# Kernel optimization log

Hardware: AMD Instinct MI355X
Metric: run time of the kernel (lower is better)

Reference implementation:

```python
import jax, jax.numpy as jnp
import numpy as np
import math

N_HEADS = 16
ROPE_THETA = 10000.0


def _rope_cos_sin(seqlen, head_dim, theta=ROPE_THETA):
    # freqs_cis = polar(1, outer(t, 1/theta^(2i/d))) -> return cos, sin parts
    inv = 1.0 / (theta ** (jnp.arange(0, head_dim, 2, dtype=jnp.float32) / head_dim))
    t = jnp.arange(seqlen, dtype=jnp.float32)
    freqs = t[:, None] * inv[None, :]          # [S, hd/2]
    return jnp.cos(freqs), jnp.sin(freqs)


def _apply_rope(x, cos, sin):
    # x: [B, S, H, hd]; treat consecutive pairs as complex, rotate by e^{i*freq}
    B, S, H, hd = x.shape
    x2 = x.astype(jnp.float32).reshape(B, S, H, hd // 2, 2)
    xr, xi = x2[..., 0], x2[..., 1]
    c = cos[None, :, None, :]
    s = sin[None, :, None, :]
    out_r = xr * c - xi * s
    out_i = xr * s + xi * c
    return jnp.stack([out_r, out_i], axis=-1).reshape(B, S, H, hd).astype(x.dtype)


def setup_inputs() -> dict:
    key = jax.random.key(0)
    ks = jax.random.split(key, 5)
    dim = 2048
    B, S = 2, 2048
    scale = 1.0 / math.sqrt(dim)
    x = jax.random.normal(ks[0], (B, S, dim), dtype=jnp.float32)
    wq = jax.random.normal(ks[1], (dim, dim), dtype=jnp.float32) * scale
    wk = jax.random.normal(ks[2], (dim, dim), dtype=jnp.float32) * scale
    wv = jax.random.normal(ks[3], (dim, dim), dtype=jnp.float32) * scale
    wo = jax.random.normal(ks[4], (dim, dim), dtype=jnp.float32) * scale
    return {"x": x, "wq": wq, "wk": wk, "wv": wv, "wo": wo}


def reference(x, wq, wk, wv, wo):
    B, S, D = x.shape
    H = N_HEADS
    hd = D // H
    # nn.Linear(bias=False): y = x @ W.T
    q = (x @ wq.T).reshape(B, S, H, hd)
    k = (x @ wk.T).reshape(B, S, H, hd)
    v = (x @ wv.T).reshape(B, S, H, hd)
    cos, sin = _rope_cos_sin(S, hd)
    q = _apply_rope(q, cos, sin)
    k = _apply_rope(k, cos, sin)
    attn = jnp.einsum('bthd,bThd->bhtT', q, k) / jnp.sqrt(jnp.float32(hd))
    attn = jax.nn.softmax(attn, axis=-1)
    out = jnp.einsum('bhtT,bThd->bthd', attn, v).reshape(B, S, D)
    return out @ wo.T
```

## Files before the change

### kernel.cpp

```cpp
#include <hip/hip_runtime.h>
#include <math.h>

typedef unsigned short u16;
typedef __bf16 bf16x8 __attribute__((ext_vector_type(8)));
typedef short s16x4 __attribute__((ext_vector_type(4)));
typedef short s16x8 __attribute__((ext_vector_type(8)));
typedef float f32x4 __attribute__((ext_vector_type(4)));

#define B_ 2
#define S_ 2048
#define D_ 2048
#define H_ 16
#define HD_ 128
#define M_ 4096
#define N3_ 6144

#define AS1(p) ((__attribute__((address_space(1))) void*)(void*)(p))
#define AS3(p) ((__attribute__((address_space(3))) void*)(p))
#define GLD16(g, l) __builtin_amdgcn_global_load_lds(AS1(g), AS3(l), 16, 0, 0)

__device__ __forceinline__ u16 f2bf(float f) {
  unsigned u = __float_as_uint(f);
  return (u16)((u + 0x7FFFu + ((u >> 16) & 1u)) >> 16);
}
__device__ __forceinline__ float bf2f(u16 v) {
  return __uint_as_float(((unsigned)v) << 16);
}

__global__ void cvt5_k(const float* __restrict__ x, const float* __restrict__ wq,
                       const float* __restrict__ wk, const float* __restrict__ wv,
                       const float* __restrict__ wo, u16* __restrict__ xb,
                       u16* __restrict__ wqkvb, u16* __restrict__ wob) {
  int y = blockIdx.y;
  const float* s;
  u16* d;
  int n4;
  if (y == 0) {
    s = x; d = xb; n4 = M_ * D_ / 4;
  } else {
    s = (y == 1) ? wq : (y == 2) ? wk : (y == 3) ? wv : wo;
    d = (y == 4) ? wob : wqkvb + (size_t)(y - 1) * D_ * D_;
    n4 = D_ * D_ / 4;
  }
  int i = blockIdx.x * 256 + threadIdx.x;
  if (i >= n4) return;
  float4 v = ((const float4*)s)[i];
  ushort4 o;
  o.x = f2bf(v.x); o.y = f2bf(v.y); o.z = f2bf(v.z); o.w = f2bf(v.w);
  ((ushort4*)d)[i] = o;
}

__global__ void rope_tab_k(float2* __restrict__ tab) {
  int t = blockIdx.x * 256 + threadIdx.x;
  if (t >= S_ * 64) return;
  int s = t >> 6, i = t & 63;
  double inv = exp2(-(double)i * (13.287712379549449 / 64.0));
  double fr = (double)s * inv;
  double sv, cv;
  sincos(fr, &sv, &cv);
  tab[t] = make_float2((float)cv, (float)sv);
}

template <typename OT>
__global__ __launch_bounds__(512, 2) void gemm256_k(const u16* __restrict__ A,
                                                    const u16* __restrict__ B,
                                                    OT* __restrict__ C,
                                                    int M, int N, int K) {
  __shared__ alignas(16) u16 sm[65536];
  const int tid = threadIdx.x;
  const int wid = tid >> 6, lane = tid & 63;
  const int quad = lane >> 4, l16 = lane & 15;
  const int wr = wid >> 2, wc = wid & 3;

  const int nby = M >> 8, nbx = N >> 8, nwg = nbx * nby;
  int bid = blockIdx.x;
  int wg = (nwg % 8 == 0) ? (bid % 8) * (nwg >> 3) + (bid >> 3) : bid;
  const int m0 = (wg % nby) << 8, n0 = (wg / nby) << 8;

  const int rr = tid >> 3;
  const int sw8 = ((tid & 7) ^ (rr & 7)) * 8;
  const int gb0 = (rr & 31) + ((rr & 32) << 1);
  const u16* pA0_0 = A + (size_t)(m0 + rr) * K + sw8;
  const u16* pA0_1 = A + (size_t)(m0 + 128 + rr) * K + sw8;
  const u16* pA1_0 = A + (size_t)(m0 + 64 + rr) * K + sw8;
  const u16* pA1_1 = A + (size_t)(m0 + 192 + rr) * K + sw8;
  const u16* pB0_0 = B + (size_t)(n0 + gb0) * K + sw8;
  const u16* pB0_1 = B + (size_t)(n0 + 128 + gb0) * K + sw8;
  const u16* pB1_0 = B + (size_t)(n0 + 32 + gb0) * K + sw8;
  const u16* pB1_1 = B + (size_t)(n0 + 160 + gb0) * K + sw8;
  const int dst0 = wid * 64 * 8, dst1 = (512 + wid * 64) * 8;

  const int pj0 = (quad ^ (l16 & 7)) * 8;
  const int pj1 = ((4 + quad) ^ (l16 & 7)) * 8;

  f32x4 acc[8][4] = {};
  const int NT = K >> 6;

  GLD16(pA0_0, sm + dst0);
  GLD16(pA0_1, sm + dst1);
  GLD16(pB0_0, sm + 32768 + dst0);
  GLD16(pB0_1, sm + 32768 + dst1);
  GLD16(pB1_0, sm + 32768 + 8192 + dst0);
  GLD16(pB1_1, sm + 32768 + 8192 + dst1);
  GLD16(pA1_0, sm + 8192 + dst0);
  GLD16(pA1_1, sm + 8192 + dst1);
  asm volatile("s_waitcnt vmcnt(4)" ::: "memory");
  asm volatile("s_barrier" ::: "memory");

  int koff = 0;
#pragma unroll 1
  for (int t = 0; t < NT; ++t) {
    const int aB = (t & 1) * 16384, bB = 32768 + (t & 1) * 16384;
    const int aN = ((t + 1) & 1) * 16384, bN = 32768 + ((t + 1) & 1) * 16384;
    const bool pre = (t + 1 < NT);
    const int kn = koff + 64;
    bf16x8 a_[4][2], b_[4][2];

#pragma unroll
    for (int m = 0; m < 4; ++m) {
      int rb = aB + (wr * 64 + m * 16 + l16) * 64;
      a_[m][0] = *(const bf16x8*)&sm[rb + pj0];
      a_[m][1] = *(const bf16x8*)&sm[rb + pj1];
    }
#pragma unroll
    for (int n = 0; n < 2; ++n) {
      int rb = bB + (wc * 32 + n * 16 + l16) * 64;
      b_[n][0] = *(const bf16x8*)&sm[rb + pj0];
      b_[n][1] = *(const bf16x8*)&sm[rb + pj1];
    }
    if (pre) { GLD16(pA0_0 + kn, sm + aN + dst0); GLD16(pA0_1 + kn, sm + aN + dst1); }
    asm volatile("s_barrier" ::: "memory");
    __builtin_amdgcn_s_setprio(1);
#pragma unroll
    for (int m = 0; m < 4; ++m)
#pragma unroll
      for (int n = 0; n < 2; ++n) {
        acc[m][n] = __builtin_amdgcn_mfma_f32_16x16x32_bf16(a_[m][0], b_[n][0], acc[m][n], 0, 0, 0);
        acc[m][n] = __builtin_amdgcn_mfma_f32_16x16x32_bf16(a_[m][1], b_[n][1], acc[m][n], 0, 0, 0);
      }
    __builtin_amdgcn_s_setprio(0);
    if (pre) asm volatile("s_waitcnt vmcnt(4)" ::: "memory");
    else     asm volatile("s_waitcnt vmcnt(0)" ::: "memory");
    asm volatile("s_barrier" ::: "memory");

#pragma unroll
    for (int n = 0; n < 2; ++n) {
      int rb = bB + (128 + wc * 32 + n * 16 + l16) * 64;
      b_[2 + n][0] = *(const bf16x8*)&sm[rb + pj0];
      b_[2 + n][1] = *(const bf16x8*)&sm[rb + pj1];
    }
    if (pre) { GLD16(pB0_0 + kn, sm + bN + dst0); GLD16(pB0_1 + kn, sm + bN + dst1); }
    asm volatile("s_barrier" ::: "memory");
    __builtin_amdgcn_s_setprio(1);
#pragma unroll
    for (int m = 0; m < 4; ++m)
#pragma unroll
      for (int n = 0; n < 2; ++n) {
        acc[m][2 + n] = __builtin_amdgcn_mfma_f32_16x16x32_bf16(a_[m][0], b_[2 + n][0], acc[m][2 + n], 0, 0, 0);
        acc[m][2 + n] = __builtin_amdgcn_mfma_f32_16x16x32_bf16(a_[m][1], b_[2 + n][1], acc[m][2 + n], 0, 0, 0);
      }
    __builtin_amdgcn_s_setprio(0);
    if (pre) asm volatile("s_waitcnt vmcnt(4)" ::: "memory");
    else     asm volatile("s_waitcnt vmcnt(0)" ::: "memory");
    asm volatile("s_barrier" ::: "memory");

#pragma unroll
    for (int m = 0; m < 4; ++m) {
      int rb = aB + (128 + wr * 64 + m * 16 + l16) * 64;
      a_[m][0] = *(const bf16x8*)&sm[rb + pj0];
      a_[m][1] = *(const bf16x8*)&sm[rb + pj1];
    }
    if (pre) { GLD16(pB1_0 + kn, sm + bN + 8192 + dst0); GLD16(pB1_1 + kn, sm + bN + 8192 + dst1); }
    asm volatile("s_barrier" ::: "memory");
    __builtin_amdgcn_s_setprio(1);
#pragma unroll
    for (int m = 0; m < 4; ++m)
#pragma unroll
      for (int n = 0; n < 2; ++n) {
        acc[4 + m][n] = __builtin_amdgcn_mfma_f32_16x16x32_bf16(a_[m][0], b_[n][0], acc[4 + m][n], 0, 0, 0);
        acc[4 + m][n] = __builtin_amdgcn_mfma_f32_16x16x32_bf16(a_[m][1], b_[n][1], acc[4 + m][n], 0, 0, 0);
      }
    __builtin_amdgcn_s_setprio(0);
    asm volatile("s_barrier" ::: "memory");

    if (pre) { GLD16(pA1_0 + kn, sm + aN + 8192 + dst0); GLD16(pA1_1 + kn, sm + aN + 8192 + dst1); }
    asm volatile("s_barrier" ::: "memory");
    __builtin_amdgcn_s_setprio(1);
#pragma unroll
    for (int m = 0; m < 4; ++m)
#pragma unroll
      for (int n = 0; n < 2; ++n) {
        acc[4 + m][2 + n] = __builtin_amdgcn_mfma_f32_16x16x32_bf16(a_[m][0], b_[2 + n][0], acc[4 + m][2 + n], 0, 0, 0);
        acc[4 + m][2 + n] = __builtin_amdgcn_mfma_f32_16x16x32_bf16(a_[m][1], b_[2 + n][1], acc[4 + m][2 + n], 0, 0, 0);
      }
    __builtin_amdgcn_s_setprio(0);
    asm volatile("s_waitcnt vmcnt(4)" ::: "memory");
    asm volatile("s_barrier" ::: "memory");
    koff = kn;
  }

#pragma unroll
  for (int m = 0; m < 8; ++m) {
#pragma unroll
    for (int n = 0; n < 4; ++n) {
      int col = n0 + wc * 64 + n * 16 + l16;
#pragma unroll
      for (int r = 0; r < 4; ++r) {
        int row = m0 + wr * 128 + m * 16 + quad * 4 + r;
        if constexpr (sizeof(OT) == 4)
          C[(size_t)row * N + col] = acc[m][n][r];
        else
          C[(size_t)row * N + col] = f2bf(acc[m][n][r]);
      }
    }
  }
}

template <typename OT>
__global__ __launch_bounds__(256) void gemm_bt_k(const u16* __restrict__ A,
                                                 const u16* __restrict__ B,
                                                 OT* __restrict__ C,
                                                 int M, int N, int K) {
  __shared__ alignas(16) u16 As[128 * 32];
  __shared__ alignas(16) u16 Bs[128 * 32];
  const int tid = threadIdx.x;
  const int wave = tid >> 6, lane = tid & 63;
  const int quad = lane >> 4, l16 = lane & 15;
  const int m0 = blockIdx.y * 128, n0 = blockIdx.x * 128;
  const int wm = (wave >> 1) * 64, wn = (wave & 1) * 64;
  const u16* Ag = A + (size_t)m0 * K;
  const u16* Bg = B + (size_t)n0 * K;
  f32x4 acc[4][4] = {};
  const int c0 = tid, c1 = tid + 256;
  const int r0 = c0 >> 2, k0b = (c0 & 3) * 8;
  const int r1 = c1 >> 2, k1b = (c1 & 3) * 8;
  u16* la0 = As + (size_t)(wave * 64) * 8;
  u16* la1 = As + (size_t)(256 + wave * 64) * 8;
  u16* lb0 = Bs + (size_t)(wave * 64) * 8;
  u16* lb1 = Bs + (size_t)(256 + wave * 64) * 8;
  for (int kt = 0; kt < K; kt += 32) {
    GLD16(Ag + (size_t)r0 * K + kt + k0b, la0);
    GLD16(Ag + (size_t)r1 * K + kt + k1b, la1);
    GLD16(Bg + (size_t)r0 * K + kt + k0b, lb0);
    GLD16(Bg + (size_t)r1 * K + kt + k1b, lb1);
    __syncthreads();
    bf16x8 af[4], bfr[4];
#pragma unroll
    for (int i = 0; i < 4; ++i)
      af[i] = *(const bf16x8*)&As[(wm + i * 16 + l16) * 32 + quad * 8];
#pragma unroll
    for (int j = 0; j < 4; ++j)
      bfr[j] = *(const bf16x8*)&Bs[(wn + j * 16 + l16) * 32 + quad * 8];
#pragma unroll
    for (int i = 0; i < 4; ++i)
#pragma unroll
      for (int j = 0; j < 4; ++j)
        acc[i][j] = __builtin_amdgcn_mfma_f32_16x16x32_bf16(af[i], bfr[j], acc[i][j], 0, 0, 0);
    __syncthreads();
  }
#pragma unroll
  for (int i = 0; i < 4; ++i) {
#pragma unroll
    for (int j = 0; j < 4; ++j) {
      int n = n0 + wn + j * 16 + l16;
#pragma unroll
      for (int r = 0; r < 4; ++r) {
        int m = m0 + wm + i * 16 + quad * 4 + r;
        if constexpr (sizeof(OT) == 4)
          C[(size_t)m * N + n] = acc[i][j][r];
        else
          C[(size_t)m * N + n] = f2bf(acc[i][j][r]);
      }
    }
  }
}

__global__ void rope_k(const u16* __restrict__ qkv, const float2* __restrict__ tab,
                       u16* __restrict__ Qr, u16* __restrict__ Kr) {
  int t = blockIdx.x * 256 + threadIdx.x;
  int m = t >> 10;
  int h = (t >> 6) & 15;
  int i = t & 63;
  int s = m & (S_ - 1);
  int b = m >> 11;
  float2 cs = tab[(s << 6) | i];
  const u16* qp = qkv + (size_t)m * N3_ + h * HD_ + 2 * i;
  ushort2 qv = *(const ushort2*)qp;
  ushort2 kv = *(const ushort2*)(qp + D_);
  float qr = bf2f(qv.x), qi = bf2f(qv.y);
  float kr = bf2f(kv.x), ki = bf2f(kv.y);
  ushort2 qo, ko;
  qo.x = f2bf(qr * cs.x - qi * cs.y);
  qo.y = f2bf(qr * cs.y + qi * cs.x);
  ko.x = f2bf(kr * cs.x - ki * cs.y);
  ko.y = f2bf(kr * cs.y + ki * cs.x);
  size_t o = ((size_t)(b * H_ + h) * S_ + s) * HD_ + 2 * i;
  *(ushort2*)(Qr + o) = qo;
  *(ushort2*)(Kr + o) = ko;
}

__global__ __launch_bounds__(256) void vperm_k(const u16* __restrict__ qkv,
                                               u16* __restrict__ Vp) {
  int bh = blockIdx.y;
  int b = bh >> 4, h = bh & 15;
  int t = blockIdx.x * 256 + threadIdx.x;
  int d = t & 127, g = t >> 7;
  const u16* src = qkv + ((size_t)(b * S_ + 4 * g)) * N3_ + 2 * D_ + h * HD_ + d;
  ushort4 o;
  o.x = src[0];
  o.y = src[N3_];
  o.z = src[2 * N3_];
  o.w = src[3 * N3_];
  *(ushort4*)(Vp + (size_t)bh * S_ * HD_ + (size_t)t * 4) = o;
}

#if __has_builtin(__builtin_amdgcn_mfma_f32_16x16x16bf16_1k)
#define HAS_MFMA16 1
#endif

__global__ __launch_bounds__(512, 2) void flash_k(const u16* __restrict__ Q,
                                                  const u16* __restrict__ Kc,
                                                  const u16* __restrict__ Vp,
                                                  u16* __restrict__ O) {
  __shared__ alignas(16) u16 sm[32768];
  const int tid = threadIdx.x;
  const int wave = tid >> 6, lane = tid & 63;
  const int quad = lane >> 4, l16 = lane & 15;
  const int qt = blockIdx.x, bh = blockIdx.y;
  const int b = bh >> 4, h = bh & 15;
  const u16* vbase_g = Vp + (size_t)bh * S_ * HD_;

#pragma unroll
  for (int i = 0; i < 8; ++i) {
    int c = i * 512 + tid, row = c >> 4, jl = c & 15;
    int gj = (jl & 8) | ((jl ^ row) & 7);
    GLD16(Q + ((size_t)bh * S_ + qt * 256 + row) * HD_ + gj * 8,
          sm + (size_t)(i * 512 + wave * 64) * 8);
  }
  __syncthreads();

  bf16x8 qf[2][4];
#pragma unroll
  for (int qs = 0; qs < 2; ++qs) {
    int row = wave * 32 + qs * 16 + l16;
#pragma unroll
    for (int dk = 0; dk < 4; ++dk) {
      int c = dk * 4 + quad, pj = (c & 8) | ((c ^ row) & 7);
      qf[qs][dk] = *(const bf16x8*)&sm[row * 128 + pj * 8];
    }
  }
  __syncthreads();

#pragma unroll
  for (int i = 0; i < 2; ++i) {
    int c = i * 512 + tid, row = c >> 4, jl = c & 15;
    int gj = (jl & 8) | ((jl ^ row) & 7);
    GLD16(Kc + ((size_t)bh * S_ + row) * HD_ + gj * 8,
          sm + 16384 + (size_t)(i * 512 + wave * 64) * 8);
    GLD16(vbase_g + (size_t)(i * 512 + tid) * 8,
          sm + 24576 + (size_t)(i * 512 + wave * 64) * 8);
  }
  __syncthreads();

  f32x4 acco[2][8] = {};
  f32x4 accl[2] = {};
  const float SCL = 0.08838834764831845f * 1.4426950408889634f;
#ifdef HAS_MFMA16
  const s16x4 ones = {(short)0x3F80, (short)0x3F80, (short)0x3F80, (short)0x3F80};
#else
  union { s16x8 s; bf16x8 b; } onesu;
  onesu.s = (s16x8){(short)0x3F80, (short)0x3F80, (short)0x3F80, (short)0x3F80,
                    (short)0x3F80, (short)0x3F80, (short)0x3F80, (short)0x3F80};
#endif

#pragma unroll 1
  for (int kt = 0; kt < 32; ++kt) {
    u16* cb = sm + ((kt & 1) ? 0 : 16384);
    u16* nb = sm + ((kt & 1) ? 16384 : 0);
    if (kt < 31) {
      const u16* vg = vbase_g + (size_t)(kt + 1) * 8192;
#pragma unroll
      for (int i = 0; i < 2; ++i) {
        int c = i * 512 + tid, row = c >> 4, jl = c & 15;
        int gj = (jl & 8) | ((jl ^ row) & 7);
        GLD16(Kc + ((size_t)bh * S_ + (kt + 1) * 64 + row) * HD_ + gj * 8,
              nb + (size_t)(i * 512 + wave * 64) * 8);
        GLD16(vg + (size_t)(i * 512 + tid) * 8,
              nb + 8192 + (size_t)(i * 512 + wave * 64) * 8);
      }
    }

    f32x4 sc[2][4] = {};
#pragma unroll
    for (int k4 = 0; k4 < 4; ++k4) {
      int row = k4 * 16 + l16;
#pragma unroll
      for (int dk = 0; dk < 4; ++dk) {
        int c = dk * 4 + quad, pj = (c & 8) | ((c ^ row) & 7);
        bf16x8 kf = *(const bf16x8*)&cb[row * 128 + pj * 8];
        sc[0][k4] = __builtin_amdgcn_mfma_f32_16x16x32_bf16(kf, qf[0][dk], sc[0][k4], 0, 0, 0);
        sc[1][k4] = __builtin_amdgcn_mfma_f32_16x16x32_bf16(kf, qf[1][dk], sc[1][k4], 0, 0, 0);
      }
    }

#ifdef HAS_MFMA16
    s16x4 ap[2][4];
#else
    bf16x8 ap[2][4];
#endif
#pragma unroll
    for (int qs = 0; qs < 2; ++qs) {
#pragma unroll
      for (int k4 = 0; k4 < 4; ++k4) {
        f32x4 s = sc[qs][k4];
        u16 p0 = f2bf(__builtin_amdgcn_exp2f(s[0] * SCL));
        u16 p1 = f2bf(__builtin_amdgcn_exp2f(s[1] * SCL));
        u16 p2 = f2bf(__builtin_amdgcn_exp2f(s[2] * SCL));
        u16 p3 = f2bf(__builtin_amdgcn_exp2f(s[3] * SCL));
#ifdef HAS_MFMA16
        ap[qs][k4] = (s16x4){(short)p0, (short)p1, (short)p2, (short)p3};
#else
        union { s16x8 s8; bf16x8 b8; } u;
        u.s8 = (s16x8){(short)p0, (short)p1, (short)p2, (short)p3, 0, 0, 0, 0};
        ap[qs][k4] = u.b8;
#endif
      }
    }

#pragma unroll
    for (int ck = 0; ck < 4; ++ck) {
      int vb = 8192 + (ck * 4 + quad) * 512 + l16 * 4;
#pragma unroll
      for (int df = 0; df < 8; ++df) {
        s16x4 bv = *(const s16x4*)&cb[vb + df * 64];
#ifdef HAS_MFMA16
        acco[0][df] = __builtin_amdgcn_mfma_f32_16x16x16bf16_1k(ap[0][ck], bv, acco[0][df], 0, 0, 0);
        acco[1][df] = __builtin_amdgcn_mfma_f32_16x16x16bf16_1k(ap[1][ck], bv, acco[1][df], 0, 0, 0);
#else
        union { s16x8 s8; bf16x8 b8; } vbu;
        vbu.s8 = (s16x8){bv[0], bv[1], bv[2], bv[3], 0, 0, 0, 0};
        acco[0][df] = __builtin_amdgcn_mfma_f32_16x16x32_bf16(ap[0][ck], vbu.b8, acco[0][df], 0, 0, 0);
        acco[1][df] = __builtin_amdgcn_mfma_f32_16x16x32_bf16(ap[1][ck], vbu.b8, acco[1][df], 0, 0, 0);
#endif
      }
#ifdef HAS_MFMA16
      accl[0] = __builtin_amdgcn_mfma_f32_16x16x16bf16_1k(ones, ap[0][ck], accl[0], 0, 0, 0);
      accl[1] = __builtin_amdgcn_mfma_f32_16x16x16bf16_1k(ones, ap[1][ck], accl[1], 0, 0, 0);
#else
      accl[0] = __builtin_amdgcn_mfma_f32_16x16x32_bf16(onesu.b, ap[0][ck], accl[0], 0, 0, 0);
      accl[1] = __builtin_amdgcn_mfma_f32_16x16x32_bf16(onesu.b, ap[1][ck], accl[1], 0, 0, 0);
#endif
    }
    __syncthreads();
  }

#pragma unroll
  for (int qs = 0; qs < 2; ++qs) {
    float lv = accl[qs][0];
    float linv[4];
#pragma unroll
    for (int r = 0; r < 4; ++r) linv[r] = 1.0f / __shfl(lv, quad * 4 + r);
    int rowb = qt * 256 + wave * 32 + qs * 16 + quad * 4;
#pragma unroll
    for (int df = 0; df < 8; ++df) {
      int col = h * HD_ + df * 16 + l16;
#pragma unroll
      for (int r = 0; r < 4; ++r)
        O[((size_t)(b * S_ + rowb + r)) * D_ + col] = f2bf(acco[qs][df][r] * linv[r]);
    }
  }
}

extern "C" void kernel_launch(void* const* d_in, const int* in_sizes, int n_in,
                              void* d_out, int out_size, void* d_ws, size_t ws_size,
                              hipStream_t stream) {
  const float* x  = (const float*)d_in[0];
  const float* wq = (const float*)d_in[1];
  const float* wk = (const float*)d_in[2];
  const float* wv = (const float*)d_in[3];
  const float* wo = (const float*)d_in[4];

  size_t off = 0;
  char* ws = (char*)d_ws;
  u16* xb    = (u16*)(ws + off); off += (size_t)M_ * D_ * 2;
  u16* wqkvb = (u16*)(ws + off); off += (size_t)3 * D_ * D_ * 2;
  u16* wob   = (u16*)(ws + off); off += (size_t)D_ * D_ * 2;
  u16* qkv   = (u16*)(ws + off); off += (size_t)M_ * N3_ * 2;
  u16* Qr    = (u16*)(ws + off); off += (size_t)M_ * D_ * 2;
  u16* Kr    = (u16*)(ws + off); off += (size_t)M_ * D_ * 2;
  u16* Vp    = (u16*)(ws + off); off += (size_t)M_ * D_ * 2;
  float2* tab = (float2*)(ws + off); off += (size_t)S_ * 64 * sizeof(float2);
  u16* Ob = qkv;
  if (off > ws_size) return;

  cvt5_k<<<dim3(M_ * D_ / 4 / 256, 5), 256, 0, stream>>>(x, wq, wk, wv, wo, xb, wqkvb, wob);
  rope_tab_k<<<(S_ * 64) / 256, 256, 0, stream>>>(tab);
  gemm256_k<u16><<<(M_ / 256) * (N3_ / 256), 512, 0, stream>>>(xb, wqkvb, qkv, M_, N3_, D_);
  rope_k<<<(M_ * H_ * 64) / 256, 256, 0, stream>>>(qkv, tab, Qr, Kr);
  vperm_k<<<dim3(S_ * HD_ / 4 / 256, B_ * H_), 256, 0, stream>>>(qkv, Vp);
  flash_k<<<dim3(S_ / 256, B_ * H_), 512, 0, stream>>>(Qr, Kr, Vp, Ob);
  gemm_bt_k<float><<<dim3(D_ / 128, M_ / 128), 256, 0, stream>>>(Ob, wob, (float*)d_out, M_, D_, D_);
}
```

Baseline: 409.9 us.

## Use 16 waves per flash block, fold softmax scale into Q rope

The flash attention kernel now launches 1024 threads (16 waves), each wave owning 16 query rows instead of 32. This halves per-wave accumulator registers and spreads the K/V tile loads over more threads. The softmax scale times log2(e) is folded into the Q rotary output so the inner loop skips a multiply, and manual bf16 rounding is replaced with native __bf16 conversions. Each wave now reuses every K/V fragment read from LDS for half as many MFMAs, and pre-scaling Q before bf16 rounding slightly changes numerics.

```diff
diff --git a/kernel.cpp b/kernel.cpp
--- a/kernel.cpp
+++ b/kernel.cpp
@@ -277,6 +277,7 @@
 
 __global__ void rope_k(const u16* __restrict__ qkv, const float2* __restrict__ tab,
                        u16* __restrict__ Qr, u16* __restrict__ Kr) {
+  const float SCLQ = 0.08838834764831845f * 1.4426950408889634f;
   int t = blockIdx.x * 256 + threadIdx.x;
   int m = t >> 10;
   int h = (t >> 6) & 15;
@@ -290,8 +291,8 @@
   float qr = bf2f(qv.x), qi = bf2f(qv.y);
   float kr = bf2f(kv.x), ki = bf2f(kv.y);
   ushort2 qo, ko;
-  qo.x = f2bf(qr * cs.x - qi * cs.y);
-  qo.y = f2bf(qr * cs.y + qi * cs.x);
+  qo.x = f2bf((qr * cs.x - qi * cs.y) * SCLQ);
+  qo.y = f2bf((qr * cs.y + qi * cs.x) * SCLQ);
   ko.x = f2bf(kr * cs.x - ki * cs.y);
   ko.y = f2bf(kr * cs.y + ki * cs.x);
   size_t o = ((size_t)(b * H_ + h) * S_ + s) * HD_ + 2 * i;
@@ -318,10 +319,10 @@
 #define HAS_MFMA16 1
 #endif
 
-__global__ __launch_bounds__(512, 2) void flash_k(const u16* __restrict__ Q,
-                                                  const u16* __restrict__ Kc,
-                                                  const u16* __restrict__ Vp,
-                                                  u16* __restrict__ O) {
+__global__ __launch_bounds__(1024, 4) void flash_k(const u16* __restrict__ Q,
+                                                   const u16* __restrict__ Kc,
+                                                   const u16* __restrict__ Vp,
+                                                   u16* __restrict__ O) {
   __shared__ alignas(16) u16 sm[32768];
   const int tid = threadIdx.x;
   const int wave = tid >> 6, lane = tid & 63;
@@ -331,40 +332,37 @@
   const u16* vbase_g = Vp + (size_t)bh * S_ * HD_;
 
 #pragma unroll
-  for (int i = 0; i < 8; ++i) {
-    int c = i * 512 + tid, row = c >> 4, jl = c & 15;
+  for (int i = 0; i < 4; ++i) {
+    int c = i * 1024 + tid, row = c >> 4, jl = c & 15;
     int gj = (jl & 8) | ((jl ^ row) & 7);
     GLD16(Q + ((size_t)bh * S_ + qt * 256 + row) * HD_ + gj * 8,
-          sm + (size_t)(i * 512 + wave * 64) * 8);
+          sm + (size_t)(i * 1024 + wave * 64) * 8);
   }
   __syncthreads();
 
-  bf16x8 qf[2][4];
-#pragma unroll
-  for (int qs = 0; qs < 2; ++qs) {
-    int row = wave * 32 + qs * 16 + l16;
+  bf16x8 qf[4];
+  {
+    int row = wave * 16 + l16;
 #pragma unroll
     for (int dk = 0; dk < 4; ++dk) {
       int c = dk * 4 + quad, pj = (c & 8) | ((c ^ row) & 7);
-      qf[qs][dk] = *(const bf16x8*)&sm[row * 128 + pj * 8];
+      qf[dk] = *(const bf16x8*)&sm[row * 128 + pj * 8];
     }
   }
   __syncthreads();
 
-#pragma unroll
-  for (int i = 0; i < 2; ++i) {
-    int c = i * 512 + tid, row = c >> 4, jl = c & 15;
+  {
+    int c = tid, row = c >> 4, jl = c & 15;
     int gj = (jl & 8) | ((jl ^ row) & 7);
     GLD16(Kc + ((size_t)bh * S_ + row) * HD_ + gj * 8,
-          sm + 16384 + (size_t)(i * 512 + wave * 64) * 8);
-    GLD16(vbase_g + (size_t)(i * 512 + tid) * 8,
-          sm + 24576 + (size_t)(i * 512 + wave * 64) * 8);
+          sm + 16384 + (size_t)(wave * 64) * 8);
+    GLD16(vbase_g + (size_t)tid * 8,
+          sm + 24576 + (size_t)(wave * 64) * 8);
   }
   __syncthreads();
 
-  f32x4 acco[2][8] = {};
-  f32x4 accl[2] = {};
-  const float SCL = 0.08838834764831845f * 1.4426950408889634f;
+  f32x4 acco[8] = {};
+  f32x4 accl = {};
 #ifdef HAS_MFMA16
   const s16x4 ones = {(short)0x3F80, (short)0x3F80, (short)0x3F80, (short)0x3F80};
 #else
@@ -378,19 +376,15 @@
     u16* cb = sm + ((kt & 1) ? 0 : 16384);
     u16* nb = sm + ((kt & 1) ? 16384 : 0);
     if (kt < 31) {
-      const u16* vg = vbase_g + (size_t)(kt + 1) * 8192;
-#pragma unroll
-      for (int i = 0; i < 2; ++i) {
-        int c = i * 512 + tid, row = c >> 4, jl = c & 15;
-        int gj = (jl & 8) | ((jl ^ row) & 7);
-        GLD16(Kc + ((size_t)bh * S_ + (kt + 1) * 64 + row) * HD_ + gj * 8,
-              nb + (size_t)(i * 512 + wave * 64) * 8);
-        GLD16(vg + (size_t)(i * 512 + tid) * 8,
-              nb + 8192 + (size_t)(i * 512 + wave * 64) * 8);
-      }
-    }
-
-    f32x4 sc[2][4] = {};
+      int c = tid, row = c >> 4, jl = c & 15;
+      int gj = (jl & 8) | ((jl ^ row) & 7);
+      GLD16(Kc + ((size_t)bh * S_ + (kt + 1) * 64 + row) * HD_ + gj * 8,
+            nb + (size_t)(wave * 64) * 8);
+      GLD16(vbase_g + (size_t)(kt + 1) * 8192 + (size_t)tid * 8,
+            nb + 8192 + (size_t)(wave * 64) * 8);
+    }
+
+    f32x4 sc[4] = {};
 #pragma unroll
     for (int k4 = 0; k4 < 4; ++k4) {
       int row = k4 * 16 + l16;
@@ -398,34 +392,36 @@
       for (int dk = 0; dk < 4; ++dk) {
         int c = dk * 4 + quad, pj = (c & 8) | ((c ^ row) & 7);
         bf16x8 kf = *(const bf16x8*)&cb[row * 128 + pj * 8];
-        sc[0][k4] = __builtin_amdgcn_mfma_f32_16x16x32_bf16(kf, qf[0][dk], sc[0][k4], 0, 0, 0);
-        sc[1][k4] = __builtin_amdgcn_mfma_f32_16x16x32_bf16(kf, qf[1][dk], sc[1][k4], 0, 0, 0);
+        sc[k4] = __builtin_amdgcn_mfma_f32_16x16x32_bf16(kf, qf[dk], sc[k4], 0, 0, 0);
       }
     }
 
 #ifdef HAS_MFMA16
-    s16x4 ap[2][4];
+    s16x4 ap[4];
+#pragma unroll
+    for (int k4 = 0; k4 < 4; ++k4) {
+      f32x4 s = sc[k4];
+      union { s16x4 s4; __bf16 bb[4]; } pu;
+      pu.bb[0] = (__bf16)__builtin_amdgcn_exp2f(s[0]);
+      pu.bb[1] = (__bf16)__builtin_amdgcn_exp2f(s[1]);
+      pu.bb[2] = (__bf16)__builtin_amdgcn_exp2f(s[2]);
+      pu.bb[3] = (__bf16)__builtin_amdgcn_exp2f(s[3]);
+      ap[k4] = pu.s4;
+    }
 #else
-    bf16x8 ap[2][4];
+    bf16x8 ap[4];
+#pragma unroll
+    for (int k4 = 0; k4 < 4; ++k4) {
+      f32x4 s = sc[k4];
+      union { s16x8 s8; bf16x8 b8; __bf16 bb[8]; } pu;
+      pu.s8 = (s16x8){0, 0, 0, 0, 0, 0, 0, 0};
+      pu.bb[0] = (__bf16)__builtin_amdgcn_exp2f(s[0]);
+      pu.bb[1] = (__bf16)__builtin_amdgcn_exp2f(s[1]);
+      pu.bb[2] = (__bf16)__builtin_amdgcn_exp2f(s[2]);
+      pu.bb[3] = (__bf16)__builtin_amdgcn_exp2f(s[3]);
+      ap[k4] = pu.b8;
+    }
 #endif
-#pragma unroll
-    for (int qs = 0; qs < 2; ++qs) {
-#pragma unroll
-      for (int k4 = 0; k4 < 4; ++k4) {
-        f32x4 s = sc[qs][k4];
-        u16 p0 = f2bf(__builtin_amdgcn_exp2f(s[0] * SCL));
-        u16 p1 = f2bf(__builtin_amdgcn_exp2f(s[1] * SCL));
-        u16 p2 = f2bf(__builtin_amdgcn_exp2f(s[2] * SCL));
-        u16 p3 = f2bf(__builtin_amdgcn_exp2f(s[3] * SCL));
-#ifdef HAS_MFMA16
-        ap[qs][k4] = (s16x4){(short)p0, (short)p1, (short)p2, (short)p3};
-#else
-        union { s16x8 s8; bf16x8 b8; } u;
-        u.s8 = (s16x8){(short)p0, (short)p1, (short)p2, (short)p3, 0, 0, 0, 0};
-        ap[qs][k4] = u.b8;
-#endif
-      }
-    }
 
 #pragma unroll
     for (int ck = 0; ck < 4; ++ck) {
@@ -434,39 +430,37 @@
       for (int df = 0; df < 8; ++df) {
         s16x4 bv = *(const s16x4*)&cb[vb + df * 64];
 #ifdef HAS_MFMA16
-        acco[0][df] = __builtin_amdgcn_mfma_f32_16x16x16bf16_1k(ap[0][ck], bv, acco[0][df], 0, 0, 0);
-        acco[1][df] = __builtin_amdgcn_mfma_f32_16x16x16bf16_1k(ap[1][ck], bv, acco[1][df], 0, 0, 0);
+        acco[df] = __builtin_amdgcn_mfma_f32_16x16x16bf16_1k(ap[ck], bv, acco[df], 0, 0, 0);
 #else
         union { s16x8 s8; bf16x8 b8; } vbu;
         vbu.s8 = (s16x8){bv[0], bv[1], bv[2], bv[3], 0, 0, 0, 0};
-        acco[0][df] = __builtin_amdgcn_mfma_f32_16x16x32_bf16(ap[0][ck], vbu.b8, acco[0][df], 0, 0, 0);
-        acco[1][df] = __builtin_amdgcn_mfma_f32_16x16x32_bf16(ap[1][ck], vbu.b8, acco[1][df], 0, 0, 0);
+        acco[df] = __builtin_amdgcn_mfma_f32_16x16x32_bf16(ap[ck], vbu.b8, acco[df], 0, 0, 0);
 #endif
       }
 #ifdef HAS_MFMA16
-      accl[0] = __builtin_amdgcn_mfma_f32_16x16x16bf16_1k(ones, ap[0][ck], accl[0], 0, 0, 0);
-      accl[1] = __builtin_amdgcn_mfma_f32_16x16x16bf16_1k(ones, ap[1][ck], accl[1], 0, 0, 0);
+      accl = __builtin_amdgcn_mfma_f32_16x16x16bf16_1k(ones, ap[ck], accl, 0, 0, 0);
 #else
-      accl[0] = __builtin_amdgcn_mfma_f32_16x16x32_bf16(onesu.b, ap[0][ck], accl[0], 0, 0, 0);
-      accl[1] = __builtin_amdgcn_mfma_f32_16x16x32_bf16(onesu.b, ap[1][ck], accl[1], 0, 0, 0);
+      accl = __builtin_amdgcn_mfma_f32_16x16x32_bf16(onesu.b, ap[ck], accl, 0, 0, 0);
 #endif
     }
     __syncthreads();
   }
 
-#pragma unroll
-  for (int qs = 0; qs < 2; ++qs) {
-    float lv = accl[qs][0];
+  {
+    float lv = accl[0];
     float linv[4];
 #pragma unroll
     for (int r = 0; r < 4; ++r) linv[r] = 1.0f / __shfl(lv, quad * 4 + r);
-    int rowb = qt * 256 + wave * 32 + qs * 16 + quad * 4;
+    int rowb = qt * 256 + wave * 16 + quad * 4;
 #pragma unroll
     for (int df = 0; df < 8; ++df) {
       int col = h * HD_ + df * 16 + l16;
 #pragma unroll
-      for (int r = 0; r < 4; ++r)
-        O[((size_t)(b * S_ + rowb + r)) * D_ + col] = f2bf(acco[qs][df][r] * linv[r]);
+      for (int r = 0; r < 4; ++r) {
+        union { u16 u; __bf16 bb; } ou;
+        ou.bb = (__bf16)(acco[df][r] * linv[r]);
+        O[((size_t)(b * S_ + rowb + r)) * D_ + col] = ou.u;
+      }
     }
   }
 }
@@ -498,6 +492,6 @@
   gemm256_k<u16><<<(M_ / 256) * (N3_ / 256), 512, 0, stream>>>(xb, wqkvb, qkv, M_, N3_, D_);
   rope_k<<<(M_ * H_ * 64) / 256, 256, 0, stream>>>(qkv, tab, Qr, Kr);
   vperm_k<<<dim3(S_ * HD_ / 4 / 256, B_ * H_), 256, 0, stream>>>(qkv, Vp);
-  flash_k<<<dim3(S_ / 256, B_ * H_), 512, 0, stream>>>(Qr, Kr, Vp, Ob);
+  flash_k<<<dim3(S_ / 256, B_ * H_), 1024, 0, stream>>>(Qr, Kr, Vp, Ob);
   gemm_bt_k<float><<<dim3(D_ / 128, M_ / 128), 256, 0, stream>>>(Ob, wob, (float*)d_out, M_, D_, D_);
 }
```

Result: no change. 410.1 us (+0.1%).
